# Optimization experiments

Hardware: AMD Instinct MI355X
Metric: run time of the kernel (lower is better)

Reference implementation:

```python
import jax, jax.numpy as jnp
import numpy as np

B = 2048       # batch
N = 256        # num_memory_locations
M = 64         # memory_size
U = 512        # num_units
IN = 10        # num_bits_per_vector + 2
SHIFT = 1      # conv_shift_range
CLIP = 20.0


def setup_inputs() -> dict:
    key = jax.random.key(0)
    ks = jax.random.split(key, 20)
    s = 0.05
    A0 = jax.random.uniform(ks[5], (2, B, N), dtype=jnp.float32)
    A0 = A0 / jnp.sum(A0, axis=-1, keepdims=True)  # distribution-like prev attention
    return {
        'x_t':  jax.random.normal(ks[0], (B, IN), dtype=jnp.float32),
        'H0':   jax.random.normal(ks[1], (B, U), dtype=jnp.float32) * s,
        'C0':   jax.random.normal(ks[2], (B, U), dtype=jnp.float32) * s,
        'm0':   jax.random.normal(ks[3], (B, N, M), dtype=jnp.float32) * s,
        'R0':   jax.random.normal(ks[4], (B, M), dtype=jnp.float32) * s,
        'A0':   A0,
        'Wprep': jax.random.normal(ks[6], (M, U), dtype=jnp.float32) * s,
        'bprep': jnp.zeros((U,), dtype=jnp.float32),
        'Wx':   jax.random.normal(ks[7], (IN + U, 4 * U), dtype=jnp.float32) * s,
        'Wh':   jax.random.normal(ks[8], (U, 4 * U), dtype=jnp.float32) * s,
        'bl':   jnp.zeros((4 * U,), dtype=jnp.float32),
        'Wr':   jax.random.normal(ks[9], (U, M + 6), dtype=jnp.float32) * s,
        'br':   jnp.zeros((M + 6,), dtype=jnp.float32),
        'Ww':   jax.random.normal(ks[10], (U, 3 * M + 6), dtype=jnp.float32) * s,
        'bw':   jnp.zeros((3 * M + 6,), dtype=jnp.float32),
        'Wo':   jax.random.normal(ks[11], (U + M, U), dtype=jnp.float32) * s,
        'bo':   jnp.zeros((U,), dtype=jnp.float32),
    }


def _addressing(head, m_tm1, a_tm1):
    # head: (B, >=M+6); m_tm1: (B,N,M); a_tm1: (B,N)
    k = jnp.tanh(head[:, :M])                                   # (B,M)
    beta = jax.nn.softplus(head[:, M])                          # (B,)
    g = jax.nn.sigmoid(head[:, M + 1])                          # (B,)
    s = jax.nn.softmax(head[:, M + 2:M + 2 + 2 * SHIFT + 1], axis=-1)  # (B,3)
    gamma = jax.nn.softplus(head[:, M + 2 + 2 * SHIFT + 1])     # (B,)
    # cosine similarity content addressing
    ip = jnp.einsum('bnm,bm->bn', m_tm1, k)                     # (B,N)
    k_norm = jnp.sqrt(jnp.sum(k * k, axis=1, keepdims=True))    # (B,1)
    m_norm = jnp.sqrt(jnp.sum(m_tm1 * m_tm1, axis=2))           # (B,N)
    K = ip / (k_norm * m_norm + 1e-8)
    w_c = jax.nn.softmax(beta[:, None] * K, axis=1)             # exp/sum == softmax
    w_g = g[:, None] * w_c + (1.0 - g[:, None]) * a_tm1
    # circular convolution: s placed at offsets [0..SHIFT] and [-SHIFT..-1]
    s_full = jnp.concatenate(
        [s[:, :SHIFT + 1], jnp.zeros((s.shape[0], N - (2 * SHIFT + 1)), s.dtype), s[:, -SHIFT:]],
        axis=1)                                                 # (B,N)
    idx = (jnp.arange(N)[:, None] - jnp.arange(N)[None, :]) % N  # (N,N)
    w_conv = jnp.einsum('bij,bj->bi', s_full[:, idx], w_g)       # w[i]=sum_j w_g[j]*s[(i-j)%N]
    w_sharp = w_conv ** gamma[:, None]
    return w_sharp / jnp.sum(w_sharp, axis=1, keepdims=True)


def reference(x_t, H0, C0, m0, R0, A0, Wprep, bprep, Wx, Wh, bl, Wr, br, Ww, bw, Wo, bo):
    # prep from previous reads
    h = R0 @ Wprep + bprep                                      # (B,U)
    # single-layer LSTM controller
    z = jnp.concatenate([x_t, h], axis=1) @ Wx + H0 @ Wh + bl   # (B,4U)
    i, f, g_, o = jnp.split(z, 4, axis=1)
    c_t = jax.nn.sigmoid(f) * C0 + jax.nn.sigmoid(i) * jnp.tanh(g_)
    h = jax.nn.sigmoid(o) * jnp.tanh(c_t)
    h = jnp.clip(h, -CLIP, CLIP)
    # heads
    r_out = h @ Wr + br                                         # (B, M+6)
    w_out = h @ Ww + bw                                         # (B, 3M+6)
    w_read = _addressing(r_out, m0, A0[0])                      # (B,N)
    w_write = _addressing(w_out, m0, A0[1])                     # (B,N)
    # read from OLD memory (as in original)
    R_t = jnp.einsum('bn,bnm->bm', w_read, m0)                  # (B,M)
    # write: erase + add
    del_v = jax.nn.sigmoid(w_out[:, -2 * M:-M])                 # (B,M)
    add_v = jnp.tanh(w_out[:, -M:])                             # (B,M)
    ww = w_write[:, :, None]                                    # (B,N,1)
    m_t = m0 * (1.0 - ww * del_v[:, None, :]) + ww * add_v[:, None, :]
    y_t = jnp.clip(jnp.concatenate([h, R_t], axis=1) @ Wo + bo, -CLIP, CLIP)
    return (y_t, m_t, R_t, w_read, w_write)
```

## Files before the change

kernel.cpp:

```cpp
#include <hip/hip_runtime.h>


using u16   = unsigned short;
using bfrag = __attribute__((ext_vector_type(8))) short;
using f4    = __attribute__((ext_vector_type(4))) float;

__device__ __forceinline__ float bf2f(u16 s){ union{float f;unsigned u;}v; v.u=((unsigned)s)<<16; return v.f; }
__device__ __forceinline__ u16 f2bf(float f){ union{float f;unsigned u;}v; v.f=f; unsigned r=v.u+0x7fffu+((v.u>>16)&1u); return (u16)(r>>16); }
__device__ __forceinline__ void bfpair(unsigned pr, float&a, float&b){ union{float f;unsigned u;}x,y; x.u=pr<<16; y.u=pr&0xffff0000u; a=x.f; b=y.f; }
__device__ __forceinline__ unsigned packbf(float a, float b){ return (unsigned)f2bf(a) | ((unsigned)f2bf(b)<<16); }
__device__ __forceinline__ float sigm(float x){ return 1.f/(1.f+expf(-x)); }
__device__ __forceinline__ float softplus_(float x){ return fmaxf(x,0.f)+log1pf(expf(-fabsf(x))); }

__device__ __forceinline__ void gld16(const u16* g, u16* l){
    __builtin_amdgcn_global_load_lds((const __attribute__((address_space(1))) unsigned*)g,
                                     (__attribute__((address_space(3))) unsigned*)l, 16, 0, 0);
}


__global__ __launch_bounds__(256) void k_wt_lstm(const float* __restrict__ Wx, const float* __restrict__ Wh,
                                                 u16* __restrict__ Wt){
    __shared__ float t[32][33];
    int n0 = blockIdx.x*32, k0 = blockIdx.y*32;
    int tx = threadIdx.x & 31, ty = threadIdx.x >> 5;
    #pragma unroll
    for(int r=0;r<4;r++){
        int k = k0 + ty*4 + r, n = n0 + tx;
        float v;
        if(k < 522)       v = Wx[k*2048 + n];
        else if(k < 1034) v = Wh[(k-522)*2048 + n];
        else              v = 0.f;
        t[ty*4+r][tx] = v;
    }
    __syncthreads();
    #pragma unroll
    for(int r=0;r<4;r++){
        int n = n0 + ty*4 + r, k = k0 + tx;
        Wt[n*1056 + k] = f2bf(t[tx][ty*4+r]);
    }
}

__global__ __launch_bounds__(256) void k_wt_heads(const float* __restrict__ Wr, const float* __restrict__ Ww,
                                                  u16* __restrict__ Wt){
    __shared__ float t[32][33];
    int n0 = blockIdx.x*32, k0 = blockIdx.y*32;
    int tx = threadIdx.x & 31, ty = threadIdx.x >> 5;
    #pragma unroll
    for(int r=0;r<4;r++){
        int k = k0 + ty*4 + r, n = n0 + tx;
        float v;
        if(n < 70)        v = Wr[k*70 + n];
        else if(n < 268)  v = Ww[k*198 + (n-70)];
        else              v = 0.f;
        t[ty*4+r][tx] = v;
    }
    __syncthreads();
    #pragma unroll
    for(int r=0;r<4;r++){
        int n = n0 + ty*4 + r, k = k0 + tx;
        Wt[n*512 + k] = f2bf(t[tx][ty*4+r]);
    }
}

__global__ __launch_bounds__(256) void k_wt_out(const float* __restrict__ Wo, u16* __restrict__ Wt){
    __shared__ float t[32][33];
    int n0 = blockIdx.x*32, k0 = blockIdx.y*32;
    int tx = threadIdx.x & 31, ty = threadIdx.x >> 5;
    #pragma unroll
    for(int r=0;r<4;r++){
        int k = k0 + ty*4 + r, n = n0 + tx;
        t[ty*4+r][tx] = Wo[k*512 + n];
    }
    __syncthreads();
    #pragma unroll
    for(int r=0;r<4;r++){
        int n = n0 + ty*4 + r, k = k0 + tx;
        Wt[n*576 + k] = f2bf(t[tx][ty*4+r]);
    }
}

__global__ __launch_bounds__(256) void k_abuild(const float* __restrict__ x, const float* __restrict__ H0,
                                                const float* __restrict__ R0, const float* __restrict__ Wprep,
                                                const float* __restrict__ bprep, u16* __restrict__ A){
    int flat = blockIdx.x*256 + threadIdx.x;
    int b = flat >> 9, u = flat & 511;
    u16* Ab = A + (size_t)b*1056;
    float acc = bprep[u];
    const float* r = R0 + b*64;
    #pragma unroll 8
    for(int m=0;m<64;m++) acc += r[m] * Wprep[m*512+u];
    Ab[10+u] = f2bf(acc);
    Ab[522+u] = f2bf(H0[b*512+u]);
    if(u<10) Ab[u] = f2bf(x[b*10+u]);
    if(u<22) Ab[1034+u] = 0;
}

__device__ __forceinline__ void gemm128(const u16* __restrict__ A, int lda,
                                        const u16* __restrict__ Bt, int ldb,
                                        int bm, int bn, int kiters,
                                        u16* Al, u16* Bl, f4 acc[4][4]){
    int tid = threadIdx.x, w = tid>>6, lane = tid&63, quad = lane>>4, l16 = lane&15;
    int wr = w>>1, wc = w&1;
    f4 z4 = {0.f,0.f,0.f,0.f};
    #pragma unroll
    for(int i=0;i<4;i++)
        #pragma unroll
        for(int j=0;j<4;j++) acc[i][j] = z4;
    int rA0 = tid>>2, kc = tid&3;
    int rA1 = rA0 + 64;
    const u16* ga0 = A  + (size_t)(bm+rA0)*lda + kc*8;
    const u16* ga1 = A  + (size_t)(bm+rA1)*lda + kc*8;
    const u16* gb0 = Bt + (size_t)(bn+rA0)*ldb + kc*8;
    const u16* gb1 = Bt + (size_t)(bn+rA1)*ldb + kc*8;
    u16* lA0 = Al + (w*64)*8;
    u16* lA1 = Al + (256 + w*64)*8;
    u16* lB0 = Bl + (w*64)*8;
    u16* lB1 = Bl + (256 + w*64)*8;
    for(int kt=0; kt<kiters; kt++){
        __syncthreads();
        gld16(ga0, lA0); gld16(ga1, lA1);
        gld16(gb0, lB0); gld16(gb1, lB1);
        ga0 += 32; ga1 += 32; gb0 += 32; gb1 += 32;
        __syncthreads();
        bfrag af[4], bf[4];
        #pragma unroll
        for(int i=0;i<4;i++) af[i] = *(const bfrag*)&Al[(wr*64 + i*16 + l16)*32 + quad*8];
        #pragma unroll
        for(int j=0;j<4;j++) bf[j] = *(const bfrag*)&Bl[(wc*64 + j*16 + l16)*32 + quad*8];
        #pragma unroll
        for(int i=0;i<4;i++)
            #pragma unroll
            for(int j=0;j<4;j++)
                acc[i][j] = __builtin_amdgcn_mfma_f32_16x16x32_bf16(af[i], bf[j], acc[i][j], 0, 0, 0);
    }
}

__global__ __launch_bounds__(256) void k_gemm_lstm(const u16* __restrict__ A, const u16* __restrict__ Wt,
                                                   float* __restrict__ z){
    __shared__ u16 Al[128*32], Bl[128*32];
    f4 acc[4][4];
    int bm = blockIdx.x*128, bn = blockIdx.y*128;
    gemm128(A, 1056, Wt, 1056, bm, bn, 33, Al, Bl, acc);
    int lane = threadIdx.x&63, quad = lane>>4, l16 = lane&15, w = threadIdx.x>>6;
    int wr = w>>1, wc = w&1;
    #pragma unroll
    for(int i=0;i<4;i++){
        #pragma unroll
        for(int j=0;j<4;j++){
            int col = bn + wc*64 + j*16 + l16;
            #pragma unroll
            for(int r=0;r<4;r++){
                int row = bm + wr*64 + i*16 + quad*4 + r;
                z[(size_t)row*2048 + col] = acc[i][j][r];
            }
        }
    }
}

__global__ __launch_bounds__(256) void k_gates(const float* __restrict__ z, const float* __restrict__ C0,
                                               const float* __restrict__ bl, u16* __restrict__ A2){
    int flat = blockIdx.x*256 + threadIdx.x;
    int b = flat>>9, u = flat&511;
    const float* zb = z + (size_t)b*2048;
    float zi = zb[u]      + bl[u];
    float zf = zb[512+u]  + bl[512+u];
    float zg = zb[1024+u] + bl[1024+u];
    float zo = zb[1536+u] + bl[1536+u];
    float c  = sigm(zf)*C0[b*512+u] + sigm(zi)*tanhf(zg);
    float hv = sigm(zo)*tanhf(c);
    hv = fminf(fmaxf(hv,-20.f),20.f);
    A2[(size_t)b*576 + u] = f2bf(hv);
}

__global__ __launch_bounds__(256) void k_gemm_heads(const u16* __restrict__ A2, const u16* __restrict__ Wt,
                                                    const float* __restrict__ br, const float* __restrict__ bw,
                                                    float* __restrict__ rout, float* __restrict__ wout){
    __shared__ u16 Al[128*32], Bl[128*32];
    f4 acc[4][4];
    int bm = blockIdx.x*128, bn = blockIdx.y*128;
    gemm128(A2, 576, Wt, 512, bm, bn, 16, Al, Bl, acc);
    int lane = threadIdx.x&63, quad = lane>>4, l16 = lane&15, w = threadIdx.x>>6;
    int wr = w>>1, wc = w&1;
    #pragma unroll
    for(int i=0;i<4;i++){
        #pragma unroll
        for(int j=0;j<4;j++){
            int col = bn + wc*64 + j*16 + l16;
            if(col >= 268) continue;
            #pragma unroll
            for(int r=0;r<4;r++){
                int row = bm + wr*64 + i*16 + quad*4 + r;
                float v = acc[i][j][r];
                if(col < 70) rout[(size_t)row*70 + col]        = v + br[col];
                else         wout[(size_t)row*198 + (col-70)]  = v + bw[col-70];
            }
        }
    }
}

__global__ __launch_bounds__(256) void k_gemm_out(const u16* __restrict__ A2, const u16* __restrict__ Wt,
                                                  const float* __restrict__ bo, float* __restrict__ y){
    __shared__ u16 Al[128*32], Bl[128*32];
    f4 acc[4][4];
    int bm = blockIdx.x*128, bn = blockIdx.y*128;
    gemm128(A2, 576, Wt, 576, bm, bn, 18, Al, Bl, acc);
    int lane = threadIdx.x&63, quad = lane>>4, l16 = lane&15, w = threadIdx.x>>6;
    int wr = w>>1, wc = w&1;
    #pragma unroll
    for(int i=0;i<4;i++){
        #pragma unroll
        for(int j=0;j<4;j++){
            int col = bn + wc*64 + j*16 + l16;
            float bias = bo[col];
            #pragma unroll
            for(int r=0;r<4;r++){
                int row = bm + wr*64 + i*16 + quad*4 + r;
                float v = acc[i][j][r] + bias;
                v = fminf(fmaxf(v,-20.f),20.f);
                y[(size_t)row*512 + col] = v;
            }
        }
    }
}

__global__ __launch_bounds__(256) void k_addr(const float* __restrict__ m0, const float* __restrict__ A0,
                                              const float* __restrict__ rout, const float* __restrict__ wout,
                                              u16* __restrict__ A2,
                                              float* __restrict__ out_mt, float* __restrict__ out_rt,
                                              float* __restrict__ out_wr, float* __restrict__ out_ww){
    __shared__ u16   m0h[256*66];
    __shared__ float kk_s[2][64];
    __shared__ float knorm_s[2];
    __shared__ float sc[2][6];
    __shared__ float wgrr[512];
    __shared__ float wsel[2][256];
    __shared__ float dv[64], avv[64];
    __shared__ float wpart[4][6];
    int tid = threadIdx.x, b = blockIdx.x;
    int lane = tid & 63, w = tid >> 6;

    float a0r = A0[b*256 + tid];
    float a1r = A0[524288 + b*256 + tid];

    const float* mb = m0 + (size_t)b*16384;
    #pragma unroll
    for(int i=0;i<16;i++){
        int e = i*1024 + tid*4;
        float4 v = *(const float4*)(mb + e);
        int n = e>>6, mc = e&63;
        unsigned* dst = (unsigned*)&m0h[n*66 + mc];
        dst[0] = packbf(v.x, v.y);
        dst[1] = packbf(v.z, v.w);
    }

    if(tid < 128){
        int hh = tid >> 6, m = lane;
        float kv = tanhf(hh ? wout[b*198 + m] : rout[b*70 + m]);
        kk_s[hh][m] = kv;
        float s2 = kv*kv;
        #pragma unroll
        for(int o=32;o>0;o>>=1) s2 += __shfl_xor(s2, o, 64);
        if(m == 0) knorm_s[hh] = sqrtf(s2);
    } else if(tid < 192){
        int hh = tid - 128;
        if(hh < 2){
            const float* hd = hh ? (wout + b*198) : (rout + b*70);
            sc[hh][0] = softplus_(hd[64]);
            sc[hh][1] = sigm(hd[65]);
            float e0=hd[66], e1=hd[67], e2=hd[68];
            float mx = fmaxf(e0, fmaxf(e1, e2));
            float x0=expf(e0-mx), x1=expf(e1-mx), x2=expf(e2-mx);
            float ssum = x0+x1+x2;
            sc[hh][2]=x0/ssum; sc[hh][3]=x1/ssum; sc[hh][4]=x2/ssum;
            sc[hh][5] = softplus_(hd[69]);
        }
    } else {
        int m = tid - 192;
        dv[m]  = sigm(wout[b*198 + 70 + m]);
        avv[m] = tanhf(wout[b*198 + 134 + m]);
    }
    __syncthreads();

    float ip0=0.f, ip1=0.f, ssq=0.f;
    {
        const u16* row = &m0h[tid*66];
        const float2* k0p = (const float2*)kk_s[0];
        const float2* k1p = (const float2*)kk_s[1];
        #pragma unroll
        for(int m=0;m<64;m+=2){
            float v0,v1; bfpair(*(const unsigned*)&row[m], v0, v1);
            float2 ka = k0p[m>>1], kb = k1p[m>>1];
            ssq += v0*v0 + v1*v1;
            ip0 += v0*ka.x + v1*ka.y;
            ip1 += v0*kb.x + v1*kb.y;
        }
    }
    float mn = sqrtf(ssq);
    float K0 = ip0 / (knorm_s[0]*mn + 1e-8f);
    float K1 = ip1 / (knorm_s[1]*mn + 1e-8f);
    float e0 = sc[0][0]*K0, e1 = sc[1][0]*K1;

    float mx0 = e0, mx1 = e1;
    #pragma unroll
    for(int o=32;o>0;o>>=1){ mx0 = fmaxf(mx0, __shfl_xor(mx0,o,64)); mx1 = fmaxf(mx1, __shfl_xor(mx1,o,64)); }
    if(lane == 0){ wpart[w][0] = mx0; wpart[w][1] = mx1; }
    __syncthreads();
    mx0 = fmaxf(fmaxf(wpart[0][0],wpart[1][0]), fmaxf(wpart[2][0],wpart[3][0]));
    mx1 = fmaxf(fmaxf(wpart[0][1],wpart[1][1]), fmaxf(wpart[2][1],wpart[3][1]));
    float p0 = expf(e0-mx0), p1 = expf(e1-mx1);
    float s0 = p0, s1 = p1;
    #pragma unroll
    for(int o=32;o>0;o>>=1){ s0 += __shfl_xor(s0,o,64); s1 += __shfl_xor(s1,o,64); }
    if(lane == 0){ wpart[w][2] = s0; wpart[w][3] = s1; }
    __syncthreads();
    s0 = wpart[0][2]+wpart[1][2]+wpart[2][2]+wpart[3][2];
    s1 = wpart[0][3]+wpart[1][3]+wpart[2][3]+wpart[3][3];
    float wc0 = p0/s0, wc1 = p1/s1;

    float g0 = sc[0][1], g1 = sc[1][1];
    float wg0 = g0*wc0 + (1.f-g0)*a0r;
    float wg1 = g1*wc1 + (1.f-g1)*a1r;
    wgrr[tid] = wg0; wgrr[256+tid] = wg1;
    __syncthreads();
    int nm1 = (tid+255)&255, np1 = (tid+1)&255;
    float conv0 = sc[0][2]*wg0 + sc[0][3]*wgrr[nm1]     + sc[0][4]*wgrr[np1];
    float conv1 = sc[1][2]*wg1 + sc[1][3]*wgrr[256+nm1] + sc[1][4]*wgrr[256+np1];
    conv0 = fmaxf(conv0, 1e-35f);  conv1 = fmaxf(conv1, 1e-35f);
    float wsh0 = expf(sc[0][5]*logf(conv0));
    float wsh1 = expf(sc[1][5]*logf(conv1));
    float t0 = wsh0, t1 = wsh1;
    #pragma unroll
    for(int o=32;o>0;o>>=1){ t0 += __shfl_xor(t0,o,64); t1 += __shfl_xor(t1,o,64); }
    if(lane == 0){ wpart[w][4] = t0; wpart[w][5] = t1; }
    __syncthreads();
    t0 = wpart[0][4]+wpart[1][4]+wpart[2][4]+wpart[3][4];
    t1 = wpart[0][5]+wpart[1][5]+wpart[2][5]+wpart[3][5];
    float w0 = wsh0/t0, w1 = wsh1/t1;
    wsel[0][tid] = w0; wsel[1][tid] = w1;
    out_wr[b*256 + tid] = w0;
    out_ww[b*256 + tid] = w1;
    __syncthreads();

    float r0=0.f, r1=0.f, r2=0.f, r3=0.f;
    {
        int mc = (tid&15)*4;
        float d0=dv[mc], d1=dv[mc+1], d2=dv[mc+2], d3=dv[mc+3];
        float A0v=avv[mc], A1v=avv[mc+1], A2v=avv[mc+2], A3v=avv[mc+3];
        float* outb = out_mt + (size_t)b*16384;
        #pragma unroll
        for(int i=0;i<16;i++){
            int e = i*1024 + tid*4;
            int n = i*16 + (tid>>4);
            float wwv = wsel[1][n], wrv = wsel[0][n];
            const unsigned* src = (const unsigned*)&m0h[n*66 + mc];
            float v0,v1,v2,v3;
            bfpair(src[0], v0, v1);
            bfpair(src[1], v2, v3);
            float4 o;
            o.x = v0*(1.f - wwv*d0) + wwv*A0v;
            o.y = v1*(1.f - wwv*d1) + wwv*A1v;
            o.z = v2*(1.f - wwv*d2) + wwv*A2v;
            o.w = v3*(1.f - wwv*d3) + wwv*A3v;
            *(float4*)(outb + e) = o;
            r0 += wrv*v0; r1 += wrv*v1; r2 += wrv*v2; r3 += wrv*v3;
        }
    }
    {
        float* rred = wgrr;
        int g = tid>>4, mc = (tid&15)*4;
        if(g >= 8){
            rred[(g-8)*64 + mc]   = r0;
            rred[(g-8)*64 + mc+1] = r1;
            rred[(g-8)*64 + mc+2] = r2;
            rred[(g-8)*64 + mc+3] = r3;
        }
        __syncthreads();
        if(g < 8){
            rred[g*64 + mc]   += r0;
            rred[g*64 + mc+1] += r1;
            rred[g*64 + mc+2] += r2;
            rred[g*64 + mc+3] += r3;
        }
        __syncthreads();
        if(tid < 64){
            float rt = 0.f;
            #pragma unroll
            for(int g2=0; g2<8; g2++) rt += rred[g2*64 + tid];
            out_rt[b*64 + tid] = rt;
            A2[(size_t)b*576 + 512 + tid] = f2bf(rt);
        }
    }
}

extern "C" void kernel_launch(void* const* d_in, const int* in_sizes, int n_in,
                              void* d_out, int out_size, void* d_ws, size_t ws_size,
                              hipStream_t stream) {
    const float* x     = (const float*)d_in[0];
    const float* H0    = (const float*)d_in[1];
    const float* C0    = (const float*)d_in[2];
    const float* m0    = (const float*)d_in[3];
    const float* R0    = (const float*)d_in[4];
    const float* A0    = (const float*)d_in[5];
    const float* Wprep = (const float*)d_in[6];
    const float* bprep = (const float*)d_in[7];
    const float* Wx    = (const float*)d_in[8];
    const float* Wh    = (const float*)d_in[9];
    const float* bl    = (const float*)d_in[10];
    const float* Wr    = (const float*)d_in[11];
    const float* br    = (const float*)d_in[12];
    const float* Ww    = (const float*)d_in[13];
    const float* bw    = (const float*)d_in[14];
    const float* Wo    = (const float*)d_in[15];
    const float* bo    = (const float*)d_in[16];

    float* ws = (float*)d_ws;
    u16*   Wt_lstm = (u16*)(ws + 0);
    u16*   Wt_h    = (u16*)(ws + 1081344);
    u16*   Wt_o    = (u16*)(ws + 1179648);
    u16*   Abuf    = (u16*)(ws + 1327104);
    u16*   A2      = (u16*)(ws + 2408448);
    float* z       =        ws + 2998272;
    float* rout    =        ws + 7192576;
    float* wout    =        ws + 7335936;

    float* out    = (float*)d_out;
    float* out_y  = out;
    float* out_mt = out + 1048576;
    float* out_rt = out + 34603008;
    float* out_wr = out + 34734080;
    float* out_ww = out + 35258368;

    hipLaunchKernelGGL(k_wt_lstm,  dim3(64,33), dim3(256), 0, stream, Wx, Wh, Wt_lstm);
    hipLaunchKernelGGL(k_wt_heads, dim3(12,16), dim3(256), 0, stream, Wr, Ww, Wt_h);
    hipLaunchKernelGGL(k_wt_out,   dim3(16,18), dim3(256), 0, stream, Wo, Wt_o);
    hipLaunchKernelGGL(k_abuild,   dim3(4096),  dim3(256), 0, stream, x, H0, R0, Wprep, bprep, Abuf);
    hipLaunchKernelGGL(k_gemm_lstm, dim3(16,16), dim3(256), 0, stream, Abuf, Wt_lstm, z);
    hipLaunchKernelGGL(k_gates,    dim3(4096),  dim3(256), 0, stream, z, C0, bl, A2);
    hipLaunchKernelGGL(k_gemm_heads, dim3(16,3), dim3(256), 0, stream, A2, Wt_h, br, bw, rout, wout);
    hipLaunchKernelGGL(k_addr,     dim3(2048),  dim3(256), 0, stream, m0, A0, rout, wout, A2,
                       out_mt, out_rt, out_wr, out_ww);
    hipLaunchKernelGGL(k_gemm_out, dim3(16,4),  dim3(256), 0, stream, A2, Wt_o, bo, out_y);
}
```

Baseline: 387.6 us.

## Drop bf16 LDS staging of memory in addressing kernel, read fp32 from global twice

The addressing kernel no longer stages each batch's 256x64 memory slice into shared memory as bf16. It reads fp32 rows straight from global memory for the cosine-similarity pass and reads them again for the erase/add write and the read-vector pass, relying on L2 for the second pass. This frees about 33 KB of LDS per block, so launch bounds now ask for 6 blocks per CU for more occupancy. The change also removes the bf16 rounding of memory, which improves accuracy, but it doubles global read traffic if the second pass misses in cache, and the per-thread row reads in the first pass are strided rather than coalesced.

After: 395.9 us. 2.1% more time.

```diff
diff --git a/kernel.cpp b/kernel.cpp
--- a/kernel.cpp
+++ b/kernel.cpp
@@ -223,35 +223,23 @@
     }
 }
 
-__global__ __launch_bounds__(256) void k_addr(const float* __restrict__ m0, const float* __restrict__ A0,
+__global__ __launch_bounds__(256, 6) void k_addr(const float* __restrict__ m0, const float* __restrict__ A0,
                                               const float* __restrict__ rout, const float* __restrict__ wout,
                                               u16* __restrict__ A2,
                                               float* __restrict__ out_mt, float* __restrict__ out_rt,
                                               float* __restrict__ out_wr, float* __restrict__ out_ww){
-    __shared__ u16   m0h[256*66];
-    __shared__ float kk_s[2][64];
+    __shared__ __align__(16) float kk_s[2][64];
     __shared__ float knorm_s[2];
     __shared__ float sc[2][6];
     __shared__ float wgrr[512];
     __shared__ float wsel[2][256];
-    __shared__ float dv[64], avv[64];
+    __shared__ __align__(16) float dv[64], avv[64];
     __shared__ float wpart[4][6];
     int tid = threadIdx.x, b = blockIdx.x;
     int lane = tid & 63, w = tid >> 6;
 
     float a0r = A0[b*256 + tid];
     float a1r = A0[524288 + b*256 + tid];
-
-    const float* mb = m0 + (size_t)b*16384;
-    #pragma unroll
-    for(int i=0;i<16;i++){
-        int e = i*1024 + tid*4;
-        float4 v = *(const float4*)(mb + e);
-        int n = e>>6, mc = e&63;
-        unsigned* dst = (unsigned*)&m0h[n*66 + mc];
-        dst[0] = packbf(v.x, v.y);
-        dst[1] = packbf(v.z, v.w);
-    }
 
     if(tid < 128){
         int hh = tid >> 6, m = lane;
@@ -283,16 +271,15 @@
 
     float ip0=0.f, ip1=0.f, ssq=0.f;
     {
-        const u16* row = &m0h[tid*66];
-        const float2* k0p = (const float2*)kk_s[0];
-        const float2* k1p = (const float2*)kk_s[1];
-        #pragma unroll
-        for(int m=0;m<64;m+=2){
-            float v0,v1; bfpair(*(const unsigned*)&row[m], v0, v1);
-            float2 ka = k0p[m>>1], kb = k1p[m>>1];
-            ssq += v0*v0 + v1*v1;
-            ip0 += v0*ka.x + v1*ka.y;
-            ip1 += v0*kb.x + v1*kb.y;
+        const float* mrow = m0 + (size_t)b*16384 + tid*64;
+        #pragma unroll
+        for(int j=0;j<16;j++){
+            float4 v  = *(const float4*)(mrow + j*4);
+            float4 ka = *(const float4*)&kk_s[0][j*4];
+            float4 kb = *(const float4*)&kk_s[1][j*4];
+            ssq += v.x*v.x + v.y*v.y + v.z*v.z + v.w*v.w;
+            ip0 += v.x*ka.x + v.y*ka.y + v.z*ka.z + v.w*ka.w;
+            ip1 += v.x*kb.x + v.y*kb.y + v.z*kb.z + v.w*kb.w;
         }
     }
     float mn = sqrtf(ssq);
@@ -346,23 +333,21 @@
         int mc = (tid&15)*4;
         float d0=dv[mc], d1=dv[mc+1], d2=dv[mc+2], d3=dv[mc+3];
         float A0v=avv[mc], A1v=avv[mc+1], A2v=avv[mc+2], A3v=avv[mc+3];
+        const float* mb = m0 + (size_t)b*16384;
         float* outb = out_mt + (size_t)b*16384;
         #pragma unroll
         for(int i=0;i<16;i++){
             int e = i*1024 + tid*4;
             int n = i*16 + (tid>>4);
             float wwv = wsel[1][n], wrv = wsel[0][n];
-            const unsigned* src = (const unsigned*)&m0h[n*66 + mc];
-            float v0,v1,v2,v3;
-            bfpair(src[0], v0, v1);
-            bfpair(src[1], v2, v3);
+            float4 v = *(const float4*)(mb + e);
             float4 o;
-            o.x = v0*(1.f - wwv*d0) + wwv*A0v;
-            o.y = v1*(1.f - wwv*d1) + wwv*A1v;
-            o.z = v2*(1.f - wwv*d2) + wwv*A2v;
-            o.w = v3*(1.f - wwv*d3) + wwv*A3v;
+            o.x = v.x*(1.f - wwv*d0) + wwv*A0v;
+            o.y = v.y*(1.f - wwv*d1) + wwv*A1v;
+            o.z = v.z*(1.f - wwv*d2) + wwv*A2v;
+            o.w = v.w*(1.f - wwv*d3) + wwv*A3v;
             *(float4*)(outb + e) = o;
-            r0 += wrv*v0; r1 += wrv*v1; r2 += wrv*v2; r3 += wrv*v3;
+            r0 += wrv*v.x; r1 += wrv*v.y; r2 += wrv*v.z; r3 += wrv*v.w;
         }
     }
     {
```
